# Optimization experiments

Hardware: AMD Instinct MI355X
Metric: run time of the kernel (lower is better)

Reference implementation:

```python
import jax, jax.numpy as jnp
import numpy as np

THETA = 10000.0


def setup_inputs() -> dict:
    key = jax.random.key(0)
    x = jax.random.normal(key, (4, 32, 4096, 128), dtype=jnp.float32)
    token_positions = jnp.arange(4096, dtype=jnp.int64)
    return {"x": x, "token_positions": token_positions}


def reference(x, token_positions):
    # Faithful RoPE: the original builds a [max_seq_len, d, d] block-diagonal
    # matrix of 2x2 rotations [[cos, -sin], [sin, cos]] over consecutive
    # (even, odd) pairs, gathers rows by token_positions, and matmuls.
    # That is mathematically identical to the pairwise rotation below.
    d = x.shape[-1]
    half = d // 2
    inv_freq = 1.0 / (THETA ** (2.0 * jnp.arange(half, dtype=jnp.float32) / d))  # [d/2]
    ang = token_positions.astype(jnp.float32)[..., None] * inv_freq  # [..., seq, d/2]
    cos = jnp.cos(ang)
    sin = jnp.sin(ang)
    xp = x.reshape(x.shape[:-1] + (half, 2))  # [..., seq, d/2, 2]
    x_even = xp[..., 0]
    x_odd = xp[..., 1]
    out_even = cos * x_even - sin * x_odd
    out_odd = sin * x_even + cos * x_odd
    out = jnp.stack([out_even, out_odd], axis=-1).reshape(x.shape)
    return out
```

## Files before the change

### kernel.cpp

```cpp
#include <hip/hip_runtime.h>
#include <math.h>


#define THETA_LOG2_OVER_HALF 0.20762050593046013f
#define FREQ_STEP 0.8659643233600653f

__global__ __launch_bounds__(256) void rope_f32_kernel(
    const float4* __restrict__ x,
    const int* __restrict__ token_positions,
    float4* __restrict__ out,
    int n4)
{
    int t = blockIdx.x * blockDim.x + threadIdx.x;
    if (t >= n4) return;

    int s  = (t >> 5) & 4095;
    int i0 = (t & 31) * 2;

    float p = (float)token_positions[s];

    float f0 = exp2f(-THETA_LOG2_OVER_HALF * (float)i0);
    float f1 = f0 * FREQ_STEP;

    float a0 = p * f0;
    float a1 = p * f1;

    float s0 = __sinf(a0), c0 = __cosf(a0);
    float s1 = __sinf(a1), c1 = __cosf(a1);

    float4 v = x[t];
    float4 r;
    r.x = c0 * v.x - s0 * v.y;
    r.y = s0 * v.x + c0 * v.y;
    r.z = c1 * v.z - s1 * v.w;
    r.w = s1 * v.z + c1 * v.w;
    out[t] = r;
}

extern "C" void kernel_launch(void* const* d_in, const int* in_sizes, int n_in,
                              void* d_out, int out_size, void* d_ws, size_t ws_size,
                              hipStream_t stream) {
    const float* x = (const float*)d_in[0];
    const int* token_positions = (const int*)d_in[1];
    float* out = (float*)d_out;

    int n4 = out_size / 4;
    int block = 256;
    int grid = (n4 + block - 1) / block;

    rope_f32_kernel<<<grid, block, 0, stream>>>(
        (const float4*)x, token_positions, (float4*)out, n4);
}
```

Measured before the change: 415.6 us.

## Precompute cos/sin table in workspace and process four float4s per thread

Adds a pre-pass kernel that computes a per-(position, frequency) cos/sin table into the workspace. The main kernel then reads that table and applies it to four float4 elements per thread, strided by a quarter of the tensor, using nontemporal loads and stores. This removes the per-element transcendental math and amortizes each table read over four batch/head slices, in exchange for an extra launch and 2MB of table traffic. The fast path depends on the workspace being large enough and the sizes being divisible; otherwise it falls back to the old kernel.

```diff
diff --git a/kernel.cpp b/kernel.cpp
--- a/kernel.cpp
+++ b/kernel.cpp
@@ -2,8 +2,80 @@
 #include <math.h>
 
 
+typedef float f32x4 __attribute__((ext_vector_type(4)));
+
 #define THETA_LOG2_OVER_HALF 0.20762050593046013f
 #define FREQ_STEP 0.8659643233600653f
+
+#define SEQ 4096
+#define ROW_F4 32
+#define TABLE_F4 (SEQ * ROW_F4)
+#define TABLE_BYTES ((size_t)TABLE_F4 * 16)
+
+__global__ __launch_bounds__(256) void rope_table_kernel(
+    const int* __restrict__ token_positions,
+    f32x4* __restrict__ table)
+{
+    int idx = blockIdx.x * blockDim.x + threadIdx.x;
+    if (idx >= TABLE_F4) return;
+    int s = idx >> 5;
+    int j = idx & 31;
+
+    float p  = (float)token_positions[s];
+    float f0 = exp2f(-THETA_LOG2_OVER_HALF * (float)(2 * j));
+    float f1 = f0 * FREQ_STEP;
+
+    float s0, c0, s1, c1;
+    sincosf(p * f0, &s0, &c0);
+    sincosf(p * f1, &s1, &c1);
+
+    f32x4 e;
+    e.x = c0; e.y = s0; e.z = c1; e.w = s1;
+    table[idx] = e;
+}
+
+__global__ __launch_bounds__(256) void rope_f32_table4_kernel(
+    const f32x4* __restrict__ x,
+    const f32x4* __restrict__ table,
+    f32x4* __restrict__ out,
+    int n4)
+{
+    int T = n4 >> 2;
+    int t = blockIdx.x * blockDim.x + threadIdx.x;
+    if (t >= T) return;
+
+    f32x4 cs = table[t & (TABLE_F4 - 1)];
+
+    f32x4 v0 = __builtin_nontemporal_load(&x[t]);
+    f32x4 v1 = __builtin_nontemporal_load(&x[t +     T]);
+    f32x4 v2 = __builtin_nontemporal_load(&x[t + 2 * T]);
+    f32x4 v3 = __builtin_nontemporal_load(&x[t + 3 * T]);
+
+    f32x4 r;
+    r.x = cs.x * v0.x - cs.y * v0.y;
+    r.y = cs.y * v0.x + cs.x * v0.y;
+    r.z = cs.z * v0.z - cs.w * v0.w;
+    r.w = cs.w * v0.z + cs.z * v0.w;
+    __builtin_nontemporal_store(r, &out[t]);
+
+    r.x = cs.x * v1.x - cs.y * v1.y;
+    r.y = cs.y * v1.x + cs.x * v1.y;
+    r.z = cs.z * v1.z - cs.w * v1.w;
+    r.w = cs.w * v1.z + cs.z * v1.w;
+    __builtin_nontemporal_store(r, &out[t + T]);
+
+    r.x = cs.x * v2.x - cs.y * v2.y;
+    r.y = cs.y * v2.x + cs.x * v2.y;
+    r.z = cs.z * v2.z - cs.w * v2.w;
+    r.w = cs.w * v2.z + cs.z * v2.w;
+    __builtin_nontemporal_store(r, &out[t + 2 * T]);
+
+    r.x = cs.x * v3.x - cs.y * v3.y;
+    r.y = cs.y * v3.x + cs.x * v3.y;
+    r.z = cs.z * v3.z - cs.w * v3.w;
+    r.w = cs.w * v3.z + cs.z * v3.w;
+    __builtin_nontemporal_store(r, &out[t + 3 * T]);
+}
 
 __global__ __launch_bounds__(256) void rope_f32_kernel(
     const float4* __restrict__ x,
@@ -17,14 +89,11 @@
     int s  = (t >> 5) & 4095;
     int i0 = (t & 31) * 2;
 
-    float p = (float)token_positions[s];
-
+    float p  = (float)token_positions[s];
     float f0 = exp2f(-THETA_LOG2_OVER_HALF * (float)i0);
     float f1 = f0 * FREQ_STEP;
 
-    float a0 = p * f0;
-    float a1 = p * f1;
-
+    float a0 = p * f0, a1 = p * f1;
     float s0 = __sinf(a0), c0 = __cosf(a0);
     float s1 = __sinf(a1), c1 = __cosf(a1);
 
@@ -40,14 +109,22 @@
 extern "C" void kernel_launch(void* const* d_in, const int* in_sizes, int n_in,
                               void* d_out, int out_size, void* d_ws, size_t ws_size,
                               hipStream_t stream) {
-    const float* x = (const float*)d_in[0];
     const int* token_positions = (const int*)d_in[1];
-    float* out = (float*)d_out;
 
     int n4 = out_size / 4;
-    int block = 256;
-    int grid = (n4 + block - 1) / block;
 
-    rope_f32_kernel<<<grid, block, 0, stream>>>(
-        (const float4*)x, token_positions, (float4*)out, n4);
+    if (ws_size >= TABLE_BYTES && n4 >= TABLE_F4 && (n4 % (TABLE_F4 * 4)) == 0) {
+        f32x4* table = (f32x4*)d_ws;
+
+        rope_table_kernel<<<dim3(TABLE_F4 / 256), dim3(256), 0, stream>>>(
+            token_positions, table);
+
+        int T = n4 >> 2;
+        rope_f32_table4_kernel<<<dim3(T / 256), dim3(256), 0, stream>>>(
+            (const f32x4*)d_in[0], table, (f32x4*)d_out, n4);
+    } else {
+        int grid = (n4 + 255) / 256;
+        rope_f32_kernel<<<grid, dim3(256), 0, stream>>>(
+            (const float4*)d_in[0], token_positions, (float4*)d_out, n4);
+    }
 }
```

After: 434.8 us. +4.6%, slower.
